# Kernel tuning notes

Measured on AMD Instinct MI355X. Metric: run time of the kernel, lower is better.

## Reference

```python
import jax, jax.numpy as jnp
import numpy as np

EMBED_DIM = 128
BATCH = 16384
HIST = 200


def setup_inputs() -> dict:
    key = jax.random.key(0)
    k1, k2, k3, k4 = jax.random.split(key, 4)
    target_embedding = jax.random.normal(k1, (BATCH, EMBED_DIM), dtype=jnp.float32)
    hist_embeddings = jax.random.normal(k2, (BATCH, HIST, EMBED_DIM), dtype=jnp.float32)
    # Dense(embedding_dim, relu): kernel [D, D], bias [D]
    W_kernel = jax.random.normal(k3, (EMBED_DIM, EMBED_DIM), dtype=jnp.float32) * (1.0 / np.sqrt(EMBED_DIM))
    W_bias = jnp.zeros((EMBED_DIM,), dtype=jnp.float32)
    # Dense(1): kernel [D, 1], bias [1]
    q_kernel = jax.random.normal(k4, (EMBED_DIM, 1), dtype=jnp.float32) * (1.0 / np.sqrt(EMBED_DIM))
    q_bias = jnp.zeros((1,), dtype=jnp.float32)
    return {
        "target_embedding": target_embedding,
        "hist_embeddings": hist_embeddings,
        "W_kernel": W_kernel,
        "W_bias": W_bias,
        "q_kernel": q_kernel,
        "q_bias": q_bias,
    }


def reference(target_embedding, hist_embeddings, W_kernel, W_bias, q_kernel, q_bias):
    # target: [B, D] -> [B, 1, D]; broadcast add with hist [B, T, D]
    x = target_embedding[:, None, :] + hist_embeddings            # [B, T, D]
    h = jax.nn.relu(jnp.einsum('btd,de->bte', x, W_kernel) + W_bias)  # [B, T, D]
    logits = jnp.einsum('btd,do->bto', h, q_kernel) + q_bias      # [B, T, 1]
    scores = jax.nn.softmax(logits, axis=1)                       # [B, T, 1]
    return jnp.sum(scores * hist_embeddings, axis=1)              # [B, D]
```

## Files before the change

### kernel.cpp

```cpp
#include <hip/hip_runtime.h>
#include <hip/hip_bf16.h>

#define D_EMB 128
#define T_HIST 200
#define T_PAD 208
#define NG 6400
#define ITERS 64
#define NBLK 256

typedef float f32x4 __attribute__((ext_vector_type(4)));
typedef short bf16x8 __attribute__((ext_vector_type(8)));

__device__ __forceinline__ short f2bf(float f) {
    unsigned u = __builtin_bit_cast(unsigned, f);
    u += 0x7fffu + ((u >> 16) & 1u);
    return (short)(u >> 16);
}

__device__ __forceinline__ float dpp_reduce16(float x) {
    int v = __builtin_bit_cast(int, x);
    x += __builtin_bit_cast(float, __builtin_amdgcn_update_dpp(0, v, 0xB1, 0xF, 0xF, true));
    v = __builtin_bit_cast(int, x);
    x += __builtin_bit_cast(float, __builtin_amdgcn_update_dpp(0, v, 0x4E, 0xF, 0xF, true));
    v = __builtin_bit_cast(int, x);
    x += __builtin_bit_cast(float, __builtin_amdgcn_update_dpp(0, v, 0x141, 0xF, 0xF, true));
    v = __builtin_bit_cast(int, x);
    x += __builtin_bit_cast(float, __builtin_amdgcn_update_dpp(0, v, 0x140, 0xF, 0xF, true));
    return x;
}

__device__ __forceinline__ uint2 cvt_granule(f32x4 v) {
    uint2 r;
    asm("v_cvt_pk_bf16_f32 %0, %1, %2" : "=v"(r.x) : "v"(v[0]), "v"(v[1]));
    asm("v_cvt_pk_bf16_f32 %0, %1, %2" : "=v"(r.y) : "v"(v[2]), "v"(v[3]));
    return r;
}

__global__ void pack_w_kernel(const float* __restrict__ W, short* __restrict__ wfrag) {
    int tid = blockIdx.x * blockDim.x + threadIdx.x;
    int fragid = tid >> 6;
    int lane = tid & 63;
    int ks = fragid >> 3;
    int nt = fragid & 7;
    int n = nt * 16 + (lane & 15);
    int k0 = ks * 32 + (lane >> 4) * 8;
    bf16x8 r;
#pragma unroll
    for (int j = 0; j < 8; ++j) r[j] = f2bf(W[(k0 + j) * D_EMB + n]);
    ((bf16x8*)wfrag)[fragid * 64 + lane] = r;
}

__global__ void tw_kernel(const float* __restrict__ target, const float* __restrict__ W,
                          const float* __restrict__ bias, float* __restrict__ TW) {
    int e = threadIdx.x;
    int b0 = blockIdx.x * 8;
    float bv = bias[e];
    float acc[8];
#pragma unroll
    for (int i = 0; i < 8; ++i) acc[i] = bv;
    for (int d = 0; d < D_EMB; ++d) {
        float wv = W[d * D_EMB + e];
#pragma unroll
        for (int i = 0; i < 8; ++i)
            acc[i] = fmaf(target[(size_t)(b0 + i) * D_EMB + d], wv, acc[i]);
    }
#pragma unroll
    for (int i = 0; i < 8; ++i) TW[(size_t)(b0 + i) * D_EMB + e] = acc[i];
}

__launch_bounds__(512, 2)
__global__ void attn_main(const float* __restrict__ hist,
                          const float* __restrict__ TW,
                          const float* __restrict__ q,
                          const short* __restrict__ wfrag,
                          float* __restrict__ out) {
    __shared__ __align__(16) uint2 h2[2][T_PAD * 32];
    __shared__ float s_tw[2][D_EMB];
    __shared__ float s_logits[2][T_PAD];
    __shared__ float s_scores[T_PAD];
    __shared__ float s_red[16];
    __shared__ float s_p2[16][D_EMB];

    const int tid = threadIdx.x;
    const int l = tid & 63;
    const int w = tid >> 6;
    const int p = w & 3;
    const int hf = w >> 2;
    const int l15 = l & 15;
    const int lg = l >> 4;
    const int r = tid >> 5;
    const int cc = tid & 31;
    const int c_log = (((cc >> 1) ^ (r & 7)) << 1) | (cc & 1);
    const int base_g = r * 32 + c_log;
    const f32x4 vzero = {0.f, 0.f, 0.f, 0.f};

    bf16x8 Bf[4][4];
#pragma unroll
    for (int ks = 0; ks < 4; ++ks)
#pragma unroll
        for (int j = 0; j < 4; ++j)
            Bf[ks][j] = ((const bf16x8*)wfrag)[(ks * 8 + hf * 4 + j) * 64 + l];

    float qv[4];
#pragma unroll
    for (int j = 0; j < 4; ++j) qv[j] = q[hf * 64 + j * 16 + l15];

    if (tid >= 256) {
        h2[0][6144 + tid] = uint2{0u, 0u};
        h2[1][6144 + tid] = uint2{0u, 0u};
    }

    const int base = blockIdx.x * ITERS;
    const f32x4* ghist = (const f32x4*)hist;

    f32x4 stgA[13], stgB[13];
    float twA = 0.f, twB = 0.f;

    {
        const f32x4* g0 = ghist + (size_t)base * NG + base_g;
#pragma unroll
        for (int k = 0; k < 12; ++k) stgA[k] = g0[k * 512];
        if (tid < 256) stgA[12] = g0[12 * 512];
        if (tid < 128) twA = TW[(size_t)base * D_EMB + tid];
        const f32x4* g1 = ghist + (size_t)(base + 1) * NG + base_g;
#pragma unroll
        for (int k = 0; k < 12; ++k) stgB[k] = g1[k * 512];
        if (tid < 256) stgB[12] = g1[12 * 512];
        if (tid < 128) twB = TW[(size_t)(base + 1) * D_EMB + tid];
    }
    {
        uint2* d = h2[0];
#pragma unroll
        for (int k = 0; k < 12; ++k) d[tid + k * 512] = cvt_granule(stgA[k]);
        if (tid < 256) d[tid + 12 * 512] = cvt_granule(stgA[12]);
        if (tid < 128) s_tw[0][tid] = twA;
    }
    __syncthreads();

#define BODY(PAR, STG_CUR, STG_OTH, TW_CUR, TW_OTH, II)                           \
    {                                                                             \
        const int bb = base + (II);                                               \
        float twv[4];                                                             \
        _Pragma("unroll") for (int j = 0; j < 4; ++j)                             \
            twv[j] = s_tw[PAR][hf * 64 + j * 16 + l15];                           \
        const bf16x8* hp = (const bf16x8*)h2[PAR];                                \
        for (int mt = p; mt < 13; mt += 4) {                                      \
            f32x4 acc[4];                                                         \
            _Pragma("unroll") for (int j = 0; j < 4; ++j) acc[j] = vzero;         \
            _Pragma("unroll") for (int ks = 0; ks < 4; ++ks) {                    \
                bf16x8 A = hp[l15 * 16 + ((ks * 4 + lg) ^ (l15 & 7)) + mt * 256]; \
                _Pragma("unroll") for (int j = 0; j < 4; ++j)                     \
                    acc[j] = __builtin_amdgcn_mfma_f32_16x16x32_bf16(             \
                        A, Bf[ks][j], acc[j], 0, 0, 0);                           \
            }                                                                     \
            float part[4] = {0.f, 0.f, 0.f, 0.f};                                 \
            _Pragma("unroll") for (int j = 0; j < 4; ++j) {                       \
                _Pragma("unroll") for (int rr = 0; rr < 4; ++rr)                  \
                    part[rr] += fmaxf(acc[j][rr] + twv[j], 0.f) * qv[j];          \
            }                                                                     \
            _Pragma("unroll") for (int rr = 0; rr < 4; ++rr)                      \
                part[rr] = dpp_reduce16(part[rr]);                                \
            if (l15 == 0) {                                                       \
                int row = mt * 16 + lg * 4;                                       \
                f32x4 v;                                                          \
                _Pragma("unroll") for (int rr = 0; rr < 4; ++rr)                  \
                    v[rr] = (row + rr < T_HIST) ? part[rr] : -1e30f;              \
                *(f32x4*)&s_logits[hf][row] = v;                                  \
            }                                                                     \
        }                                                                         \
               \
        if ((II) + 1 < ITERS) {                                                   \
            uint2* d = h2[1 - (PAR)];                                             \
            _Pragma("unroll") for (int k = 0; k < 12; ++k)                        \
                d[tid + k * 512] = cvt_granule(STG_OTH[k]);                       \
            if (tid < 256) d[tid + 12 * 512] = cvt_granule(STG_OTH[12]);          \
            if (tid < 128) s_tw[1 - (PAR)][tid] = TW_OTH;                         \
        }                                                                         \
        __syncthreads();                                                          \
        float lv = (tid < T_PAD) ? (s_logits[0][tid] + s_logits[1][tid]) : -1e30f;\
        float m = lv;                                                             \
        _Pragma("unroll") for (int off = 32; off >= 1; off >>= 1)                 \
            m = fmaxf(m, __shfl_xor(m, off, 64));                                 \
        if (l == 0) s_red[w] = m;                                                 \
        __syncthreads();                                                          \
        float M = s_red[0];                                                       \
        _Pragma("unroll") for (int k = 1; k < 8; ++k) M = fmaxf(M, s_red[k]);     \
        float e = (tid < T_PAD) ? __expf(lv - M) : 0.f;                           \
        if (tid < T_PAD) s_scores[tid] = e;                                       \
        float sm = e;                                                             \
        _Pragma("unroll") for (int off = 32; off >= 1; off >>= 1)                 \
            sm += __shfl_xor(sm, off, 64);                                        \
        if (l == 0) s_red[8 + w] = sm;                                            \
        __syncthreads();                                                          \
        float S = s_red[8];                                                       \
        _Pragma("unroll") for (int k = 9; k < 16; ++k) S += s_red[k];             \
                                             \
        f32x4 acc2 = vzero;                                                       \
        _Pragma("unroll") for (int k = 0; k < 12; ++k) {                          \
            float sc = s_scores[r + 16 * k];                                      \
            _Pragma("unroll") for (int rr = 0; rr < 4; ++rr)                      \
                acc2[rr] = fmaf(sc, STG_CUR[k][rr], acc2[rr]);                    \
        }                                                                         \
        if (tid < 256) {                                                          \
            float sc = s_scores[r + 192];                                         \
            _Pragma("unroll") for (int rr = 0; rr < 4; ++rr)                      \
                acc2[rr] = fmaf(sc, STG_CUR[12][rr], acc2[rr]);                   \
        }                                                                         \
        *(f32x4*)&s_p2[r][c_log * 4] = acc2;                                      \
        __syncthreads();                                                          \
        if (tid < 128) {                                                          \
            float o = 0.f;                                                        \
            _Pragma("unroll") for (int k = 0; k < 16; ++k) o += s_p2[k][tid];     \
            out[(size_t)bb * D_EMB + tid] = o / S;                                \
        }                                                                         \
            \
        if ((II) + 2 < ITERS) {                                                   \
            const f32x4* gn = ghist + (size_t)(bb + 2) * NG + base_g;             \
            _Pragma("unroll") for (int k = 0; k < 12; ++k) STG_CUR[k] = gn[k*512];\
            if (tid < 256) STG_CUR[12] = gn[12 * 512];                            \
            if (tid < 128) TW_CUR = TW[(size_t)(bb + 2) * D_EMB + tid];           \
        }                                                                         \
    }

    for (int ii = 0; ii < ITERS; ii += 2) {
        BODY(0, stgA, stgB, twA, twB, ii)
        BODY(1, stgB, stgA, twB, twA, ii + 1)
    }
#undef BODY
}

extern "C" void kernel_launch(void* const* d_in, const int* in_sizes, int n_in,
                              void* d_out, int out_size, void* d_ws, size_t ws_size,
                              hipStream_t stream) {
    const float* target = (const float*)d_in[0];
    const float* hist   = (const float*)d_in[1];
    const float* Wk     = (const float*)d_in[2];
    const float* Wb     = (const float*)d_in[3];
    const float* qk     = (const float*)d_in[4];
    float* out = (float*)d_out;

    short* wfrag = (short*)d_ws;
    float* TW    = (float*)((char*)d_ws + 32768);

    pack_w_kernel<<<dim3(8), dim3(256), 0, stream>>>(Wk, wfrag);
    tw_kernel<<<dim3(2048), dim3(128), 0, stream>>>(target, Wk, Wb, TW);
    attn_main<<<dim3(NBLK), dim3(512), 0, stream>>>(hist, TW, qk, wfrag, out);
}
```

Baseline: 366.5 us.

## Use lgkm-only barriers and reorder LDS staging after global prefetch

Replaces __syncthreads with a custom barrier that waits only on LDS counters (lgkmcnt) and not on outstanding global loads, so prefetched global reads stay in flight across barriers. The conversion of the next tile into LDS moves after the issue of the following prefetch, with an extra barrier at the end of each body. Loads are made unconditional (clamped index for the tail row, tid&127 for TW) so the memory ops are not predicated. The extra barrier per iteration and the reordering could add sync cost or change how well memory latency is hidden.

Result: slower. 447.7 us (+22.2%).

```diff
diff --git a/kernel.cpp b/kernel.cpp
--- a/kernel.cpp
+++ b/kernel.cpp
@@ -15,6 +15,12 @@
     unsigned u = __builtin_bit_cast(unsigned, f);
     u += 0x7fffu + ((u >> 16) & 1u);
     return (short)(u >> 16);
+}
+
+__device__ __forceinline__ void wg_barrier() {
+    asm volatile("s_waitcnt lgkmcnt(0)" ::: "memory");
+    __builtin_amdgcn_s_barrier();
+    __builtin_amdgcn_sched_barrier(0);
 }
 
 __device__ __forceinline__ float dpp_reduce16(float x) {
@@ -92,6 +98,7 @@
     const int cc = tid & 31;
     const int c_log = (((cc >> 1) ^ (r & 7)) << 1) | (cc & 1);
     const int base_g = r * 32 + c_log;
+    const int idx12 = (tid < 256) ? base_g + 12 * 512 : 0;
     const f32x4 vzero = {0.f, 0.f, 0.f, 0.f};
 
     bf16x8 Bf[4][4];
@@ -114,19 +121,19 @@
     const f32x4* ghist = (const f32x4*)hist;
 
     f32x4 stgA[13], stgB[13];
-    float twA = 0.f, twB = 0.f;
+    float twA, twB;
 
     {
-        const f32x4* g0 = ghist + (size_t)base * NG + base_g;
-#pragma unroll
-        for (int k = 0; k < 12; ++k) stgA[k] = g0[k * 512];
-        if (tid < 256) stgA[12] = g0[12 * 512];
-        if (tid < 128) twA = TW[(size_t)base * D_EMB + tid];
-        const f32x4* g1 = ghist + (size_t)(base + 1) * NG + base_g;
-#pragma unroll
-        for (int k = 0; k < 12; ++k) stgB[k] = g1[k * 512];
-        if (tid < 256) stgB[12] = g1[12 * 512];
-        if (tid < 128) twB = TW[(size_t)(base + 1) * D_EMB + tid];
+        const f32x4* g0 = ghist + (size_t)base * NG;
+#pragma unroll
+        for (int k = 0; k < 12; ++k) stgA[k] = g0[base_g + k * 512];
+        stgA[12] = g0[idx12];
+        twA = TW[(size_t)base * D_EMB + (tid & 127)];
+        const f32x4* g1 = ghist + (size_t)(base + 1) * NG;
+#pragma unroll
+        for (int k = 0; k < 12; ++k) stgB[k] = g1[base_g + k * 512];
+        stgB[12] = g1[idx12];
+        twB = TW[(size_t)(base + 1) * D_EMB + (tid & 127)];
     }
     {
         uint2* d = h2[0];
@@ -135,7 +142,7 @@
         if (tid < 256) d[tid + 12 * 512] = cvt_granule(stgA[12]);
         if (tid < 128) s_tw[0][tid] = twA;
     }
-    __syncthreads();
+    wg_barrier();
 
 #define BODY(PAR, STG_CUR, STG_OTH, TW_CUR, TW_OTH, II)                           \
     {                                                                             \
@@ -168,21 +175,13 @@
                 *(f32x4*)&s_logits[hf][row] = v;                                  \
             }                                                                     \
         }                                                                         \
-               \
-        if ((II) + 1 < ITERS) {                                                   \
-            uint2* d = h2[1 - (PAR)];                                             \
-            _Pragma("unroll") for (int k = 0; k < 12; ++k)                        \
-                d[tid + k * 512] = cvt_granule(STG_OTH[k]);                       \
-            if (tid < 256) d[tid + 12 * 512] = cvt_granule(STG_OTH[12]);          \
-            if (tid < 128) s_tw[1 - (PAR)][tid] = TW_OTH;                         \
-        }                                                                         \
-        __syncthreads();                                                          \
+        wg_barrier();                                                             \
         float lv = (tid < T_PAD) ? (s_logits[0][tid] + s_logits[1][tid]) : -1e30f;\
         float m = lv;                                                             \
         _Pragma("unroll") for (int off = 32; off >= 1; off >>= 1)                 \
             m = fmaxf(m, __shfl_xor(m, off, 64));                                 \
         if (l == 0) s_red[w] = m;                                                 \
-        __syncthreads();                                                          \
+        wg_barrier();                                                             \
         float M = s_red[0];                                                       \
         _Pragma("unroll") for (int k = 1; k < 8; ++k) M = fmaxf(M, s_red[k]);     \
         float e = (tid < T_PAD) ? __expf(lv - M) : 0.f;                           \
@@ -191,10 +190,10 @@
         _Pragma("unroll") for (int off = 32; off >= 1; off >>= 1)                 \
             sm += __shfl_xor(sm, off, 64);                                        \
         if (l == 0) s_red[8 + w] = sm;                                            \
-        __syncthreads();                                                          \
+        wg_barrier();                                                             \
         float S = s_red[8];                                                       \
         _Pragma("unroll") for (int k = 9; k < 16; ++k) S += s_red[k];             \
-                                             \
+                                   \
         f32x4 acc2 = vzero;                                                       \
         _Pragma("unroll") for (int k = 0; k < 12; ++k) {                          \
             float sc = s_scores[r + 16 * k];                                      \
@@ -207,19 +206,30 @@
                 acc2[rr] = fmaf(sc, STG_CUR[12][rr], acc2[rr]);                   \
         }                                                                         \
         *(f32x4*)&s_p2[r][c_log * 4] = acc2;                                      \
-        __syncthreads();                                                          \
+        wg_barrier();                                                             \
         if (tid < 128) {                                                          \
             float o = 0.f;                                                        \
             _Pragma("unroll") for (int k = 0; k < 16; ++k) o += s_p2[k][tid];     \
             out[(size_t)bb * D_EMB + tid] = o / S;                                \
         }                                                                         \
-            \
+             \
         if ((II) + 2 < ITERS) {                                                   \
-            const f32x4* gn = ghist + (size_t)(bb + 2) * NG + base_g;             \
-            _Pragma("unroll") for (int k = 0; k < 12; ++k) STG_CUR[k] = gn[k*512];\
-            if (tid < 256) STG_CUR[12] = gn[12 * 512];                            \
-            if (tid < 128) TW_CUR = TW[(size_t)(bb + 2) * D_EMB + tid];           \
-        }                                                                         \
+            const f32x4* gn = ghist + (size_t)(bb + 2) * NG;                      \
+            _Pragma("unroll") for (int k = 0; k < 12; ++k)                        \
+                STG_CUR[k] = gn[base_g + k * 512];                                \
+            STG_CUR[12] = gn[idx12];                                              \
+            TW_CUR = TW[(size_t)(bb + 2) * D_EMB + (tid & 127)];                  \
+        }                                                                         \
+              \
+                      \
+        if ((II) + 1 < ITERS) {                                                   \
+            uint2* d = h2[1 - (PAR)];                                             \
+            _Pragma("unroll") for (int k = 0; k < 12; ++k)                        \
+                d[tid + k * 512] = cvt_granule(STG_OTH[k]);                       \
+            if (tid < 256) d[tid + 12 * 512] = cvt_granule(STG_OTH[12]);          \
+            if (tid < 128) s_tw[1 - (PAR)][tid] = TW_OTH;                         \
+        }                                                                         \
+        wg_barrier();                                                             \
     }
 
     for (int ii = 0; ii < ITERS; ii += 2) {
```
